# Performance work log

Measured on AMD Instinct MI355X. Metric: run time of the kernel, lower is better.

Reference implementation:

```python
import jax, jax.numpy as jnp
import numpy as np

DECAY = 0.6
GAIN = 0.4


def _layernorm(x, g, b, eps=1e-5):
    m = x.mean(-1, keepdims=True)
    v = x.var(-1, keepdims=True)
    return (x - m) * jax.lax.rsqrt(v + eps) * g + b


def _ema_scan(x, axis, reverse=False):
    # linear recurrence state = 0.6*state + 0.4*x as an associative scan
    a = jnp.full_like(x, DECAY)
    b = GAIN * x
    def comb(c1, c2):
        a1, b1 = c1
        a2, b2 = c2
        return a1 * a2, a2 * b1 + b2
    _, y = jax.lax.associative_scan(comb, (a, b), axis=axis, reverse=reverse)
    return y


def setup_inputs() -> dict:
    key = jax.random.key(0)
    B, H, W, D = 16, 64, 64, 384
    inner = 2 * D
    hidden = 4 * D
    ks = jax.random.split(key, 12)
    s = 0.02
    return {
        "x": jax.random.normal(ks[0], (B, H, W, D), jnp.float32),
        "n1_g": jnp.ones((D,), jnp.float32),
        "n1_b": jnp.zeros((D,), jnp.float32),
        "w_in": s * jax.random.normal(ks[1], (D, inner), jnp.float32),
        "b_in": jnp.zeros((inner,), jnp.float32),
        "k_conv": s * jax.random.normal(ks[2], (3, 3, 1, inner), jnp.float32),  # depthwise HWIO
        "on_g": jnp.ones((inner,), jnp.float32),
        "on_b": jnp.zeros((inner,), jnp.float32),
        "w_out": s * jax.random.normal(ks[3], (inner, D), jnp.float32),
        "b_out": jnp.zeros((D,), jnp.float32),
        "n2_g": jnp.ones((D,), jnp.float32),
        "n2_b": jnp.zeros((D,), jnp.float32),
        "w1": s * jax.random.normal(ks[4], (D, hidden), jnp.float32),
        "b1": jnp.zeros((hidden,), jnp.float32),
        "w2": s * jax.random.normal(ks[5], (hidden, D), jnp.float32),
        "b2": jnp.zeros((D,), jnp.float32),
    }


def reference(x, n1_g, n1_b, w_in, b_in, k_conv, on_g, on_b, w_out, b_out,
              n2_g, n2_b, w1, b1, w2, b2):
    inner = w_in.shape[1]
    # --- LegacyScan2DOperator branch ---
    h = _layernorm(x, n1_g, n1_b)
    p = h @ w_in + b_in  # [B,H,W,inner]
    local = jax.lax.conv_general_dilated(
        p, k_conv, window_strides=(1, 1), padding="SAME",
        dimension_numbers=("NHWC", "HWIO", "NHWC"),
        feature_group_count=inner)
    lr = _ema_scan(local, axis=2)                 # left->right over W
    rl = _ema_scan(local, axis=2, reverse=True)   # right->left
    tb = _ema_scan(local, axis=1)                 # top->bottom over H
    bt = _ema_scan(local, axis=1, reverse=True)   # bottom->top
    mixed = 0.25 * (lr + rl + tb + bt) + local
    mixed = _layernorm(mixed, on_g, on_b)
    x = x + (mixed @ w_out + b_out)
    # --- MLP branch ---
    h2 = _layernorm(x, n2_g, n2_b)
    m = jax.nn.gelu(h2 @ w1 + b1, approximate=False) @ w2 + b2
    return x + m
```

## Files before the change

kernel.cpp:

```cpp
#include <hip/hip_runtime.h>
#include <math.h>


typedef __attribute__((ext_vector_type(8))) short bf16x8;
typedef __attribute__((ext_vector_type(4))) float f32x4;

#define T_TOKENS 65536
#define DMODEL 384
#define DINNER 768
#define DHIDDEN 1536

__device__ __forceinline__ float bf2f(unsigned short u) {
  unsigned int x = ((unsigned int)u) << 16;
  return __builtin_bit_cast(float, x);
}
__device__ __forceinline__ unsigned short f2bf(float f) {
  unsigned int x = __builtin_bit_cast(unsigned int, f);
  x += 0x7fffu + ((x >> 16) & 1u);
  return (unsigned short)(x >> 16);
}
__device__ __forceinline__ void unpack2(unsigned int u, float& lo, float& hi) {
  lo = __builtin_bit_cast(float, u << 16);
  hi = __builtin_bit_cast(float, u & 0xffff0000u);
}
__device__ __forceinline__ unsigned int pack2(float lo, float hi) {
  return (unsigned int)f2bf(lo) | ((unsigned int)f2bf(hi) << 16);
}

__device__ __forceinline__ void gload16(const void* g, void* l) {
  __builtin_amdgcn_global_load_lds(
      (const __attribute__((address_space(1))) void*)g,
      (__attribute__((address_space(3))) void*)l, 16, 0, 0);
}

__global__ __launch_bounds__(256) void ln_fused_f32_384(
    const float* __restrict__ in, const float* __restrict__ g,
    const float* __restrict__ b, unsigned short* __restrict__ out) {
  const int tok = blockIdx.x * 4 + (threadIdx.x >> 6);
  const int lane = threadIdx.x & 63;
  const float2* row = (const float2*)(in + (size_t)tok * 384);
  float2 v[3];
  float s = 0.f, ss = 0.f;
#pragma unroll
  for (int k = 0; k < 3; k++) {
    v[k] = row[lane + 64 * k];
    s += v[k].x + v[k].y;
    ss += v[k].x * v[k].x + v[k].y * v[k].y;
  }
#pragma unroll
  for (int off = 32; off > 0; off >>= 1) {
    s += __shfl_xor(s, off);
    ss += __shfl_xor(ss, off);
  }
  const float m = s * (1.0f / 384.0f);
  const float r = rsqrtf(ss * (1.0f / 384.0f) - m * m + 1e-5f);
  unsigned int* op = (unsigned int*)(out + (size_t)tok * 384);
#pragma unroll
  for (int k = 0; k < 3; k++) {
    const int c = lane + 64 * k;
    const float2 gg = ((const float2*)g)[c];
    const float2 bb = ((const float2*)b)[c];
    op[c] = pack2((v[k].x - m) * r * gg.x + bb.x, (v[k].y - m) * r * gg.y + bb.y);
  }
}

__global__ __launch_bounds__(256) void ln_bundle_768(
    const uint4* __restrict__ mixed, const float* __restrict__ g,
    const float* __restrict__ b, uint4* __restrict__ out) {
  const int bb_ = blockIdx.x >> 4, pg = blockIdx.x & 15;
  const int pos = pg * 256 + threadIdx.x;
  const size_t slab = (size_t)bb_ * 4096 + pos;
  float s = 0.f, ss = 0.f;
#pragma unroll 1
  for (int cg = 0; cg < 96; cg++) {
    const uint4 v = mixed[(size_t)cg * 16 * 4096 + slab];
    float e0, e1, e2, e3, e4, e5, e6, e7;
    unpack2(v.x, e0, e1); unpack2(v.y, e2, e3);
    unpack2(v.z, e4, e5); unpack2(v.w, e6, e7);
    s += (e0 + e1) + (e2 + e3) + (e4 + e5) + (e6 + e7);
    ss += e0 * e0 + e1 * e1 + e2 * e2 + e3 * e3 + e4 * e4 + e5 * e5 +
          e6 * e6 + e7 * e7;
  }
  const float m = s * (1.0f / 768.0f);
  const float r = rsqrtf(ss * (1.0f / 768.0f) - m * m + 1e-5f);
  const size_t tokbase = ((size_t)bb_ * 4096 + pos) * (768 / 8);
#pragma unroll 1
  for (int cq = 0; cq < 24; cq++) {
#pragma unroll
    for (int j = 0; j < 4; j++) {
      const int cg = cq * 4 + j;
      const uint4 v = mixed[(size_t)cg * 16 * 4096 + slab];
      const float4 g0 = *(const float4*)(g + cg * 8);
      const float4 g1 = *(const float4*)(g + cg * 8 + 4);
      const float4 b0 = *(const float4*)(b + cg * 8);
      const float4 b1 = *(const float4*)(b + cg * 8 + 4);
      float e0, e1, e2, e3, e4, e5, e6, e7;
      unpack2(v.x, e0, e1); unpack2(v.y, e2, e3);
      unpack2(v.z, e4, e5); unpack2(v.w, e6, e7);
      uint4 o;
      o.x = pack2((e0 - m) * r * g0.x + b0.x, (e1 - m) * r * g0.y + b0.y);
      o.y = pack2((e2 - m) * r * g0.z + b0.z, (e3 - m) * r * g0.w + b0.w);
      o.z = pack2((e4 - m) * r * g1.x + b1.x, (e5 - m) * r * g1.y + b1.y);
      o.w = pack2((e6 - m) * r * g1.z + b1.z, (e7 - m) * r * g1.w + b1.w);
      out[tokbase + cq * 4 + j] = o;
    }
  }
}

__global__ __launch_bounds__(256) void wprep_kernel(const float* __restrict__ in,
                                                    unsigned short* __restrict__ out,
                                                    int K, int N) {
  __shared__ float t[32][33];
  const int k0 = blockIdx.x * 32, n0 = blockIdx.y * 32;
  const int a = threadIdx.x & 31, b8 = threadIdx.x >> 5;
#pragma unroll
  for (int i = 0; i < 4; i++)
    t[b8 + 8 * i][a] = in[(size_t)(k0 + b8 + 8 * i) * N + n0 + a];
  __syncthreads();
#pragma unroll
  for (int i = 0; i < 4; i++)
    out[(size_t)(n0 + b8 + 8 * i) * K + k0 + a] = f2bf(t[a][b8 + 8 * i]);
}

template <int EPI>
__global__ __launch_bounds__(256) void gemm_bt_kernel(
    const unsigned short* __restrict__ A, int lda,
    const unsigned short* __restrict__ Bt, int ldb, int KT,
    const float* __restrict__ bias, const float* __restrict__ res,
    void* __restrict__ C, int ldc, int nby) {
  __shared__ unsigned short smem[32768];
  char* const smc = (char*)smem;

  const int tid = threadIdx.x;
  const int w = tid >> 6, lane = tid & 63;
  const int cpx = gridDim.x >> 3;
  const int g = blockIdx.x;
  const int sw = (g & 7) * cpx + (g >> 3);
  const int bx = sw / nby, by = sw - bx * nby;
  const int tok0 = bx << 7, n0 = by << 7;

  const int wm = w >> 1, wn = w & 1;
  const int lrow = lane & 15, kgrp = lane >> 4;
  const int cx = lrow & 7;

  const int lr8 = lane >> 3;
  const int kce = ((lane & 7) ^ lr8) << 3;
  const unsigned short* Abase = A + (size_t)(tok0 + w * 32 + lr8) * lda + kce;
  const unsigned short* Bbase = Bt + (size_t)(n0 + w * 32 + lr8) * ldb + kce;

  f32x4 acc[4][4];
#pragma unroll
  for (int i = 0; i < 4; i++)
#pragma unroll
    for (int j = 0; j < 4; j++) {
      f32x4 z = {0.f, 0.f, 0.f, 0.f};
      acc[i][j] = z;
    }

  const int nt = KT >> 6;
#pragma unroll
  for (int i = 0; i < 4; i++) {
    gload16(Abase + (size_t)i * 8 * lda, smc + (w * 4 + i) * 1024);
    gload16(Bbase + (size_t)i * 8 * ldb, smc + 32768 + (w * 4 + i) * 1024);
  }
  __syncthreads();

  int buf = 0;
  for (int t = 0; t < nt; t++) {
    if (t + 1 < nt) {
      const int kt = (t + 1) << 6;
      const int bo = (buf ^ 1) * 16384;
#pragma unroll
      for (int i = 0; i < 4; i++) {
        gload16(Abase + (size_t)i * 8 * lda + kt, smc + bo + (w * 4 + i) * 1024);
        gload16(Bbase + (size_t)i * 8 * ldb + kt,
                smc + 32768 + bo + (w * 4 + i) * 1024);
      }
    }
    bf16x8 af[2][4], bf_[2][4];
    const int bo = buf * 16384;
#pragma unroll
    for (int ks = 0; ks < 2; ks++) {
#pragma unroll
      for (int f = 0; f < 4; f++) {
        const int co = ((ks * 4 + kgrp) ^ cx) << 4;
        af[ks][f] =
            *(const bf16x8*)(smc + bo + (wm * 64 + f * 16 + lrow) * 128 + co);
        bf_[ks][f] = *(const bf16x8*)(smc + 32768 + bo +
                                      (wn * 64 + f * 16 + lrow) * 128 + co);
      }
    }
#pragma unroll
    for (int ks = 0; ks < 2; ks++)
#pragma unroll
      for (int mf = 0; mf < 4; mf++)
#pragma unroll
        for (int nf = 0; nf < 4; nf++)
          acc[mf][nf] = __builtin_amdgcn_mfma_f32_16x16x32_bf16(
              af[ks][mf], bf_[ks][nf], acc[mf][nf], 0, 0, 0);
    __syncthreads();
    buf ^= 1;
  }

  if constexpr (EPI == 3) {
#pragma unroll
    for (int mf = 0; mf < 4; mf++)
#pragma unroll
      for (int nf = 0; nf < 4; nf++) {
        const int cl = wn * 64 + nf * 16 + lrow;
        const float bv = bias[n0 + cl];
#pragma unroll
        for (int r = 0; r < 4; r++) {
          const int tl = wm * 64 + mf * 16 + kgrp * 4 + r;
          smem[(cl >> 3) * 1032 + tl * 8 + (cl & 7)] =
              f2bf(acc[mf][nf][r] + bv);
        }
      }
    __syncthreads();
    const int bb_ = tok0 >> 12, pos0 = tok0 & 4095, cg0 = n0 >> 3;
    uint4* Cb = (uint4*)C;
#pragma unroll
    for (int e = 0; e < 8; e++) {
      const int lin = e * 256 + tid;
      const int cgl = lin >> 7, pp = lin & 127;
      const uint4 v = *(const uint4*)&smem[cgl * 1032 + pp * 8];
      Cb[((size_t)(cg0 + cgl) * 16 + bb_) * 4096 + pos0 + pp] = v;
    }
  } else {
#pragma unroll
    for (int mf = 0; mf < 4; mf++) {
#pragma unroll
      for (int nf = 0; nf < 4; nf++) {
        const int gcol = n0 + wn * 64 + nf * 16 + lrow;
        const float bv = bias ? bias[gcol] : 0.0f;
#pragma unroll
        for (int r = 0; r < 4; r++) {
          const int grow = tok0 + wm * 64 + mf * 16 + kgrp * 4 + r;
          float v = acc[mf][nf][r] + bv;
          const size_t idx = (size_t)grow * ldc + gcol;
          if constexpr (EPI == 1) {
            ((float*)C)[idx] = v + res[idx];
          } else {
            const float z = 1.5957691216057308f * (v + 0.044715f * v * v * v);
            const float gl = v / (1.0f + __expf(-z));
            ((unsigned short*)C)[idx] = f2bf(gl);
          }
        }
      }
    }
  }
}

__global__ __launch_bounds__(256) void conv_scan_kernel(
    const uint4* __restrict__ p, const float* __restrict__ kconv,
    uint4* __restrict__ mixed) {
  __shared__ unsigned int loc[4][64][65];
  const int tid = threadIdx.x;
  const int cg = blockIdx.x;
  const int b = blockIdx.y;
  const uint4* pb = p + ((size_t)cg * 16 + b) * 4096;

  {
    float kw[9][8];
#pragma unroll
    for (int t = 0; t < 9; t++) {
      const float4 ka = *(const float4*)(kconv + t * DINNER + cg * 8);
      const float4 kb = *(const float4*)(kconv + t * DINNER + cg * 8 + 4);
      kw[t][0] = ka.x; kw[t][1] = ka.y; kw[t][2] = ka.z; kw[t][3] = ka.w;
      kw[t][4] = kb.x; kw[t][5] = kb.y; kw[t][6] = kb.z; kw[t][7] = kb.w;
    }
#pragma unroll 1
    for (int i = 0; i < 16; i++) {
      const int pos = tid + 256 * i;
      const int h = pos >> 6, w = pos & 63;
      float acc[8];
#pragma unroll
      for (int j = 0; j < 8; j++) acc[j] = 0.f;
#pragma unroll
      for (int dh = 0; dh < 3; dh++) {
        const int hh = h + dh - 1;
        const bool vh = (unsigned)hh < 64u;
        const int hcl = min(max(hh, 0), 63);
#pragma unroll
        for (int dw = 0; dw < 3; dw++) {
          const int ww = w + dw - 1;
          const bool vv = vh && ((unsigned)ww < 64u);
          const int wcl = min(max(ww, 0), 63);
          uint4 pv = pb[hcl * 64 + wcl];
          if (!vv) { pv.x = 0; pv.y = 0; pv.z = 0; pv.w = 0; }
          const int t = dh * 3 + dw;
          float lo, hi;
          unpack2(pv.x, lo, hi); acc[0] += lo * kw[t][0]; acc[1] += hi * kw[t][1];
          unpack2(pv.y, lo, hi); acc[2] += lo * kw[t][2]; acc[3] += hi * kw[t][3];
          unpack2(pv.z, lo, hi); acc[4] += lo * kw[t][4]; acc[5] += hi * kw[t][5];
          unpack2(pv.w, lo, hi); acc[6] += lo * kw[t][6]; acc[7] += hi * kw[t][7];
        }
      }
      loc[0][h][w] = pack2(acc[0], acc[1]);
      loc[1][h][w] = pack2(acc[2], acc[3]);
      loc[2][h][w] = pack2(acc[4], acc[5]);
      loc[3][h][w] = pack2(acc[6], acc[7]);
    }
  }
  __syncthreads();

  const int ax = tid & 63;
  const int cp = tid >> 6;

  unsigned int hc[64];
  {
    float ya = 0.f, yb = 0.f;
#pragma unroll
    for (int h = 0; h < 64; h++) {
      float a, bv;
      unpack2(loc[cp][h][ax], a, bv);
      ya = 0.6f * ya + 0.4f * a;
      yb = 0.6f * yb + 0.4f * bv;
      hc[h] = pack2(ya, yb);
    }
    ya = 0.f; yb = 0.f;
#pragma unroll
    for (int h = 63; h >= 0; h--) {
      float a, bv, fa, fb;
      unpack2(loc[cp][h][ax], a, bv);
      ya = 0.6f * ya + 0.4f * a;
      yb = 0.6f * yb + 0.4f * bv;
      unpack2(hc[h], fa, fb);
      hc[h] = pack2(0.25f * (fa + ya), 0.25f * (fb + yb));
    }
  }
  unsigned int wt[64];
  {
    float ya = 0.f, yb = 0.f;
#pragma unroll
    for (int w = 0; w < 64; w++) {
      float a, bv;
      unpack2(loc[cp][ax][w], a, bv);
      ya = 0.6f * ya + 0.4f * a;
      yb = 0.6f * yb + 0.4f * bv;
      wt[w] = pack2(ya, yb);
    }
    ya = 0.f; yb = 0.f;
#pragma unroll
    for (int w = 63; w >= 0; w--) {
      float a, bv, fa, fb;
      unpack2(loc[cp][ax][w], a, bv);
      ya = 0.6f * ya + 0.4f * a;
      yb = 0.6f * yb + 0.4f * bv;
      unpack2(wt[w], fa, fb);
      wt[w] = pack2(a + 0.25f * (fa + ya), bv + 0.25f * (fb + yb));
    }
  }
  __syncthreads();
#pragma unroll
  for (int w = 0; w < 64; w++) loc[cp][ax][w] = wt[w];
  __syncthreads();
#pragma unroll
  for (int h = 0; h < 64; h++) {
    float a, bv, ca, cb;
    unpack2(loc[cp][h][ax], a, bv);
    unpack2(hc[h], ca, cb);
    loc[cp][h][ax] = pack2(a + ca, bv + cb);
  }
  __syncthreads();
  uint4* mb = mixed + ((size_t)cg * 16 + b) * 4096;
#pragma unroll 1
  for (int i = 0; i < 16; i++) {
    const int pos = tid + 256 * i;
    const int h = pos >> 6, w = pos & 63;
    uint4 st;
    st.x = loc[0][h][w];
    st.y = loc[1][h][w];
    st.z = loc[2][h][w];
    st.w = loc[3][h][w];
    mb[pos] = st;
  }
}

extern "C" void kernel_launch(void* const* d_in, const int* in_sizes, int n_in,
                              void* d_out, int out_size, void* d_ws,
                              size_t ws_size, hipStream_t stream) {
  const float* x = (const float*)d_in[0];
  const float* n1_g = (const float*)d_in[1];
  const float* n1_b = (const float*)d_in[2];
  const float* w_in = (const float*)d_in[3];
  const float* b_in = (const float*)d_in[4];
  const float* k_conv = (const float*)d_in[5];
  const float* on_g = (const float*)d_in[6];
  const float* on_b = (const float*)d_in[7];
  const float* w_out = (const float*)d_in[8];
  const float* b_out = (const float*)d_in[9];
  const float* n2_g = (const float*)d_in[10];
  const float* n2_b = (const float*)d_in[11];
  const float* w1 = (const float*)d_in[12];
  const float* b1 = (const float*)d_in[13];
  const float* w2 = (const float*)d_in[14];
  const float* b2 = (const float*)d_in[15];

  const size_t MB = 1024 * 1024;
  char* ws = (char*)d_ws;
  unsigned short* R1 = (unsigned short*)(ws + 3 * MB / 2);
  unsigned short* R2 = (unsigned short*)(ws + 3 * MB / 2 + 96 * MB);

  unsigned short* A1 = R2;
  unsigned short* wTin = R2 + (48 * MB) / 2;
  unsigned short* p = R1;
  unsigned short* A2 = R2;
  unsigned short* wTout = R1;
  unsigned short* A3 = R1;
  unsigned short* wT1 = R1 + (48 * MB) / 2;
  unsigned short* wT2 = wT1 + (size_t)1536 * 384;
  unsigned short* gb = R2;

  float* out = (float*)d_out;
  dim3 b256(256);

  ln_fused_f32_384<<<T_TOKENS / 4, b256, 0, stream>>>(x, n1_g, n1_b, A1);
  wprep_kernel<<<dim3(12, 24), b256, 0, stream>>>(w_in, wTin, DMODEL, DINNER);
  gemm_bt_kernel<3><<<3072, b256, 0, stream>>>(A1, DMODEL, wTin, DMODEL, DMODEL,
                                               b_in, nullptr, p, DINNER, 6);
  conv_scan_kernel<<<dim3(96, 16), b256, 0, stream>>>(
      (const uint4*)p, k_conv, (uint4*)p);
  ln_bundle_768<<<256, b256, 0, stream>>>((const uint4*)p, on_g, on_b,
                                          (uint4*)A2);
  wprep_kernel<<<dim3(24, 12), b256, 0, stream>>>(w_out, wTout, DINNER, DMODEL);
  gemm_bt_kernel<1><<<1536, b256, 0, stream>>>(A2, DINNER, wTout, DINNER, DINNER,
                                               b_out, x, out, DMODEL, 3);
  ln_fused_f32_384<<<T_TOKENS / 4, b256, 0, stream>>>(out, n2_g, n2_b, A3);
  wprep_kernel<<<dim3(12, 48), b256, 0, stream>>>(w1, wT1, DMODEL, DHIDDEN);
  wprep_kernel<<<dim3(48, 12), b256, 0, stream>>>(w2, wT2, DHIDDEN, DMODEL);
  for (int hh = 0; hh < 2; hh++) {
    const size_t toff = (size_t)hh * 32768;
    gemm_bt_kernel<2><<<3072, b256, 0, stream>>>(
        A3 + toff * DMODEL, DMODEL, wT1, DMODEL, DMODEL, b1, nullptr, gb,
        DHIDDEN, 12);
    gemm_bt_kernel<1><<<768, b256, 0, stream>>>(
        gb, DHIDDEN, wT2, DHIDDEN, DHIDDEN, b2, out + toff * DMODEL,
        out + toff * DMODEL, DMODEL, 3);
  }
}
```

Before: 749.9 us.

## Split conv-scan into parallel H/W scan groups and widen LayerNorm-768 grid

The conv+scan kernel now runs 512 threads per block. One half does the vertical scans and the other half does the horizontal scans concurrently, and the barriers are rearranged so the W-scan results land in shared memory before the H-scan results are added. The conv taps are staged in LDS instead of registers, which frees registers for the larger block. The 768-wide LayerNorm kernel now assigns four threads per token with shuffle reductions and launches 1024 blocks instead of 256, exposing more parallelism for that memory-bound pass. The cost is extra barrier complexity, mismatched __syncthreads counts across the divergent branches, and register pressure under the (512,4) launch bounds.

```diff
diff --git a/kernel.cpp b/kernel.cpp
--- a/kernel.cpp
+++ b/kernel.cpp
@@ -67,13 +67,15 @@
 __global__ __launch_bounds__(256) void ln_bundle_768(
     const uint4* __restrict__ mixed, const float* __restrict__ g,
     const float* __restrict__ b, uint4* __restrict__ out) {
-  const int bb_ = blockIdx.x >> 4, pg = blockIdx.x & 15;
-  const int pos = pg * 256 + threadIdx.x;
-  const size_t slab = (size_t)bb_ * 4096 + pos;
+  const int tid = threadIdx.x;
+  const int tk = tid >> 2, j = tid & 3;
+  const int token = blockIdx.x * 64 + tk;
+  const int bb_ = token >> 12, posb = token & 4095;
+  const size_t slab = (size_t)bb_ * 4096 + posb;
   float s = 0.f, ss = 0.f;
 #pragma unroll 1
-  for (int cg = 0; cg < 96; cg++) {
-    const uint4 v = mixed[(size_t)cg * 16 * 4096 + slab];
+  for (int cg = j; cg < 96; cg += 4) {
+    const uint4 v = mixed[((size_t)cg * 16) * 4096 + slab];
     float e0, e1, e2, e3, e4, e5, e6, e7;
     unpack2(v.x, e0, e1); unpack2(v.y, e2, e3);
     unpack2(v.z, e4, e5); unpack2(v.w, e6, e7);
@@ -81,29 +83,27 @@
     ss += e0 * e0 + e1 * e1 + e2 * e2 + e3 * e3 + e4 * e4 + e5 * e5 +
           e6 * e6 + e7 * e7;
   }
+  s += __shfl_xor(s, 1); ss += __shfl_xor(ss, 1);
+  s += __shfl_xor(s, 2); ss += __shfl_xor(ss, 2);
   const float m = s * (1.0f / 768.0f);
   const float r = rsqrtf(ss * (1.0f / 768.0f) - m * m + 1e-5f);
-  const size_t tokbase = ((size_t)bb_ * 4096 + pos) * (768 / 8);
+  const size_t tokbase = (size_t)token * 96;
 #pragma unroll 1
-  for (int cq = 0; cq < 24; cq++) {
-#pragma unroll
-    for (int j = 0; j < 4; j++) {
-      const int cg = cq * 4 + j;
-      const uint4 v = mixed[(size_t)cg * 16 * 4096 + slab];
-      const float4 g0 = *(const float4*)(g + cg * 8);
-      const float4 g1 = *(const float4*)(g + cg * 8 + 4);
-      const float4 b0 = *(const float4*)(b + cg * 8);
-      const float4 b1 = *(const float4*)(b + cg * 8 + 4);
-      float e0, e1, e2, e3, e4, e5, e6, e7;
-      unpack2(v.x, e0, e1); unpack2(v.y, e2, e3);
-      unpack2(v.z, e4, e5); unpack2(v.w, e6, e7);
-      uint4 o;
-      o.x = pack2((e0 - m) * r * g0.x + b0.x, (e1 - m) * r * g0.y + b0.y);
-      o.y = pack2((e2 - m) * r * g0.z + b0.z, (e3 - m) * r * g0.w + b0.w);
-      o.z = pack2((e4 - m) * r * g1.x + b1.x, (e5 - m) * r * g1.y + b1.y);
-      o.w = pack2((e6 - m) * r * g1.z + b1.z, (e7 - m) * r * g1.w + b1.w);
-      out[tokbase + cq * 4 + j] = o;
-    }
+  for (int cg = j; cg < 96; cg += 4) {
+    const uint4 v = mixed[((size_t)cg * 16) * 4096 + slab];
+    const float4 g0 = *(const float4*)(g + cg * 8);
+    const float4 g1 = *(const float4*)(g + cg * 8 + 4);
+    const float4 b0 = *(const float4*)(b + cg * 8);
+    const float4 b1 = *(const float4*)(b + cg * 8 + 4);
+    float e0, e1, e2, e3, e4, e5, e6, e7;
+    unpack2(v.x, e0, e1); unpack2(v.y, e2, e3);
+    unpack2(v.z, e4, e5); unpack2(v.w, e6, e7);
+    uint4 o;
+    o.x = pack2((e0 - m) * r * g0.x + b0.x, (e1 - m) * r * g0.y + b0.y);
+    o.y = pack2((e2 - m) * r * g0.z + b0.z, (e3 - m) * r * g0.w + b0.w);
+    o.z = pack2((e4 - m) * r * g1.x + b1.x, (e5 - m) * r * g1.y + b1.y);
+    o.w = pack2((e6 - m) * r * g1.z + b1.z, (e7 - m) * r * g1.w + b1.w);
+    out[tokbase + cg] = o;
   }
 }
 
@@ -251,64 +251,64 @@
   }
 }
 
-__global__ __launch_bounds__(256) void conv_scan_kernel(
+__global__ __launch_bounds__(512, 4) void conv_scan_kernel(
     const uint4* __restrict__ p, const float* __restrict__ kconv,
     uint4* __restrict__ mixed) {
   __shared__ unsigned int loc[4][64][65];
+  __shared__ float klds[72];
   const int tid = threadIdx.x;
   const int cg = blockIdx.x;
   const int b = blockIdx.y;
   const uint4* pb = p + ((size_t)cg * 16 + b) * 4096;
 
-  {
-    float kw[9][8];
-#pragma unroll
-    for (int t = 0; t < 9; t++) {
-      const float4 ka = *(const float4*)(kconv + t * DINNER + cg * 8);
-      const float4 kb = *(const float4*)(kconv + t * DINNER + cg * 8 + 4);
-      kw[t][0] = ka.x; kw[t][1] = ka.y; kw[t][2] = ka.z; kw[t][3] = ka.w;
-      kw[t][4] = kb.x; kw[t][5] = kb.y; kw[t][6] = kb.z; kw[t][7] = kb.w;
-    }
+  if (tid < 72) klds[tid] = kconv[(tid >> 3) * DINNER + cg * 8 + (tid & 7)];
+  __syncthreads();
+
 #pragma unroll 1
-    for (int i = 0; i < 16; i++) {
-      const int pos = tid + 256 * i;
-      const int h = pos >> 6, w = pos & 63;
-      float acc[8];
-#pragma unroll
-      for (int j = 0; j < 8; j++) acc[j] = 0.f;
-#pragma unroll
-      for (int dh = 0; dh < 3; dh++) {
-        const int hh = h + dh - 1;
-        const bool vh = (unsigned)hh < 64u;
-        const int hcl = min(max(hh, 0), 63);
-#pragma unroll
-        for (int dw = 0; dw < 3; dw++) {
-          const int ww = w + dw - 1;
-          const bool vv = vh && ((unsigned)ww < 64u);
-          const int wcl = min(max(ww, 0), 63);
-          uint4 pv = pb[hcl * 64 + wcl];
-          if (!vv) { pv.x = 0; pv.y = 0; pv.z = 0; pv.w = 0; }
-          const int t = dh * 3 + dw;
-          float lo, hi;
-          unpack2(pv.x, lo, hi); acc[0] += lo * kw[t][0]; acc[1] += hi * kw[t][1];
-          unpack2(pv.y, lo, hi); acc[2] += lo * kw[t][2]; acc[3] += hi * kw[t][3];
-          unpack2(pv.z, lo, hi); acc[4] += lo * kw[t][4]; acc[5] += hi * kw[t][5];
-          unpack2(pv.w, lo, hi); acc[6] += lo * kw[t][6]; acc[7] += hi * kw[t][7];
-        }
+  for (int i = 0; i < 8; i++) {
+    const int pos = tid + 512 * i;
+    const int h = pos >> 6, w = pos & 63;
+    float acc[8];
+#pragma unroll
+    for (int j = 0; j < 8; j++) acc[j] = 0.f;
+#pragma unroll
+    for (int dh = 0; dh < 3; dh++) {
+      const int hh = h + dh - 1;
+      const bool vh = (unsigned)hh < 64u;
+      const int hcl = min(max(hh, 0), 63);
+#pragma unroll
+      for (int dw = 0; dw < 3; dw++) {
+        const int ww = w + dw - 1;
+        const bool vv = vh && ((unsigned)ww < 64u);
+        const int wcl = min(max(ww, 0), 63);
+        uint4 pv = pb[hcl * 64 + wcl];
+        if (!vv) { pv.x = 0; pv.y = 0; pv.z = 0; pv.w = 0; }
+        const int t = dh * 3 + dw;
+        float lo, hi;
+        unpack2(pv.x, lo, hi);
+        acc[0] += lo * klds[t * 8 + 0]; acc[1] += hi * klds[t * 8 + 1];
+        unpack2(pv.y, lo, hi);
+        acc[2] += lo * klds[t * 8 + 2]; acc[3] += hi * klds[t * 8 + 3];
+        unpack2(pv.z, lo, hi);
+        acc[4] += lo * klds[t * 8 + 4]; acc[5] += hi * klds[t * 8 + 5];
+        unpack2(pv.w, lo, hi);
+        acc[6] += lo * klds[t * 8 + 6]; acc[7] += hi * klds[t * 8 + 7];
       }
-      loc[0][h][w] = pack2(acc[0], acc[1]);
-      loc[1][h][w] = pack2(acc[2], acc[3]);
-      loc[2][h][w] = pack2(acc[4], acc[5]);
-      loc[3][h][w] = pack2(acc[6], acc[7]);
-    }
+    }
+    loc[0][h][w] = pack2(acc[0], acc[1]);
+    loc[1][h][w] = pack2(acc[2], acc[3]);
+    loc[2][h][w] = pack2(acc[4], acc[5]);
+    loc[3][h][w] = pack2(acc[6], acc[7]);
   }
   __syncthreads();
 
-  const int ax = tid & 63;
-  const int cp = tid >> 6;
-
-  unsigned int hc[64];
-  {
+  const int grp = tid >> 8;
+  const int r_ = tid & 255;
+  const int ax = r_ & 63;
+  const int cp = r_ >> 6;
+
+  if (grp == 0) {
+    unsigned int hc[64];
     float ya = 0.f, yb = 0.f;
 #pragma unroll
     for (int h = 0; h < 64; h++) {
@@ -328,9 +328,17 @@
       unpack2(hc[h], fa, fb);
       hc[h] = pack2(0.25f * (fa + ya), 0.25f * (fb + yb));
     }
-  }
-  unsigned int wt[64];
-  {
+    __syncthreads();
+    __syncthreads();
+#pragma unroll
+    for (int h = 0; h < 64; h++) {
+      float a, bv, ca, cb;
+      unpack2(loc[cp][h][ax], a, bv);
+      unpack2(hc[h], ca, cb);
+      loc[cp][h][ax] = pack2(a + ca, bv + cb);
+    }
+  } else {
+    unsigned int wt[64];
     float ya = 0.f, yb = 0.f;
 #pragma unroll
     for (int w = 0; w < 64; w++) {
@@ -350,23 +358,17 @@
       unpack2(wt[w], fa, fb);
       wt[w] = pack2(a + 0.25f * (fa + ya), bv + 0.25f * (fb + yb));
     }
+    __syncthreads();
+#pragma unroll
+    for (int w = 0; w < 64; w++) loc[cp][ax][w] = wt[w];
+    __syncthreads();
   }
   __syncthreads();
-#pragma unroll
-  for (int w = 0; w < 64; w++) loc[cp][ax][w] = wt[w];
-  __syncthreads();
-#pragma unroll
-  for (int h = 0; h < 64; h++) {
-    float a, bv, ca, cb;
-    unpack2(loc[cp][h][ax], a, bv);
-    unpack2(hc[h], ca, cb);
-    loc[cp][h][ax] = pack2(a + ca, bv + cb);
-  }
-  __syncthreads();
+
   uint4* mb = mixed + ((size_t)cg * 16 + b) * 4096;
 #pragma unroll 1
-  for (int i = 0; i < 16; i++) {
-    const int pos = tid + 256 * i;
+  for (int i = 0; i < 8; i++) {
+    const int pos = tid + 512 * i;
     const int h = pos >> 6, w = pos & 63;
     uint4 st;
     st.x = loc[0][h][w];
@@ -419,10 +421,10 @@
   wprep_kernel<<<dim3(12, 24), b256, 0, stream>>>(w_in, wTin, DMODEL, DINNER);
   gemm_bt_kernel<3><<<3072, b256, 0, stream>>>(A1, DMODEL, wTin, DMODEL, DMODEL,
                                                b_in, nullptr, p, DINNER, 6);
-  conv_scan_kernel<<<dim3(96, 16), b256, 0, stream>>>(
+  conv_scan_kernel<<<dim3(96, 16), dim3(512), 0, stream>>>(
       (const uint4*)p, k_conv, (uint4*)p);
-  ln_bundle_768<<<256, b256, 0, stream>>>((const uint4*)p, on_g, on_b,
-                                          (uint4*)A2);
+  ln_bundle_768<<<1024, b256, 0, stream>>>((const uint4*)p, on_g, on_b,
+                                           (uint4*)A2);
   wprep_kernel<<<dim3(24, 12), b256, 0, stream>>>(w_out, wTout, DINNER, DMODEL);
   gemm_bt_kernel<1><<<1536, b256, 0, stream>>>(A2, DINNER, wTout, DINNER, DINNER,
                                                b_out, x, out, DMODEL, 3);
```

After: 1.167 ms. +55.6%, slower.
